# Performance work log

Hardware: AMD Instinct MI355X
Metric: run time of the kernel (lower is better)

The kernel has to match this reference:

```python
import jax, jax.numpy as jnp
import numpy as np

B, T, C, H = 4, 2048, 1024, 16


def setup_inputs() -> dict:
    key = jax.random.key(0)
    k1, k2, k3 = jax.random.split(key, 3)
    x = jax.random.normal(k1, (B, T, C), dtype=jnp.float32)
    Wqkv = jax.random.normal(k2, (C, 3 * C), dtype=jnp.float32) * 0.02
    bqkv = jnp.zeros((3 * C,), dtype=jnp.float32)
    Wproj = jax.random.normal(k3, (C, C), dtype=jnp.float32) * 0.02
    bproj = jnp.zeros((C,), dtype=jnp.float32)
    return {"x": x, "Wqkv": Wqkv, "bqkv": bqkv, "Wproj": Wproj, "bproj": bproj}


def reference(x, Wqkv, bqkv, Wproj, bproj):
    Bx, Tx, Cx = x.shape
    head = Cx // H
    qkv = x @ Wqkv + bqkv                      # [B,T,3C]
    q, k, v = jnp.split(qkv, 3, axis=-1)
    q = q.reshape(Bx, Tx, H, head)
    k = k.reshape(Bx, Tx, H, head)
    v = v.reshape(Bx, Tx, H, head)
    scale = 1.0 / jnp.sqrt(jnp.asarray(head, dtype=x.dtype))
    scores = jnp.einsum('bqhd,bkhd->bhqk', q, k) * scale   # [B,H,T,T]
    causal = jnp.tril(jnp.ones((Tx, Tx), dtype=bool))       # [T,T]
    neg = jnp.finfo(x.dtype).min
    scores = jnp.where(causal[None, None, :, :], scores, neg)
    probs = jax.nn.softmax(scores, axis=-1)
    y = jnp.einsum('bhqk,bkhd->bqhd', probs, v).reshape(Bx, Tx, Cx)
    return y @ Wproj + bproj
```

## Files before the change

kernel.cpp:

```cpp
#include <hip/hip_runtime.h>
#include <stdint.h>

#define BB 4
#define TT 2048
#define CC 1024
#define HH 16

typedef __bf16 bf16x8 __attribute__((ext_vector_type(8)));
typedef float f32x4 __attribute__((ext_vector_type(4)));
typedef float f32x16 __attribute__((ext_vector_type(16)));
typedef unsigned short ushort8 __attribute__((ext_vector_type(8)));
typedef unsigned short ushort4v __attribute__((ext_vector_type(4)));

__device__ __forceinline__ unsigned short f2b(float f) {
    union { float f; unsigned u; } v; v.f = f;
    unsigned r = v.u + 0x7FFFu + ((v.u >> 16) & 1u);
    return (unsigned short)(r >> 16);
}
__device__ __forceinline__ unsigned pack2(float a, float b) {
    union { float f; unsigned u; } ua, ub; ua.f = a; ub.f = b;
    return __builtin_amdgcn_perm(ub.u + 0x8000u, ua.u + 0x8000u, 0x07060302u);
}
__device__ __forceinline__ float fexp2(float x) {
#if __has_builtin(__builtin_amdgcn_exp2f)
    return __builtin_amdgcn_exp2f(x);
#else
    return exp2f(x);
#endif
}
#define LOG2E 1.4426950408889634f

#define ASYNC16(gp, lp) __builtin_amdgcn_global_load_lds( \
    (const __attribute__((address_space(1))) void*)(gp),  \
    (__attribute__((address_space(3))) void*)(lp), 16, 0, 0)

__global__ __launch_bounds__(256) void k_prep(const float* __restrict__ x,
                                              unsigned short* __restrict__ x16,
                                              const float* __restrict__ Wqkv,
                                              unsigned short* __restrict__ wqkvT,
                                              const float* __restrict__ Wproj,
                                              unsigned short* __restrict__ wprojT) {
    const int bid = blockIdx.x;
    const int t = threadIdx.x;
    if (bid < 8192) {
        int i = (bid * 256 + t) * 4;
        float4 v = *(const float4*)(x + i);
        ushort4v o;
        o.x = f2b(v.x); o.y = f2b(v.y); o.z = f2b(v.z); o.w = f2b(v.w);
        *(ushort4v*)(x16 + i) = o;
        return;
    }
    __shared__ float tile[32][33];
    const float* in; unsigned short* out; int R, Cc, bx, by;
    if (bid < 11264) {
        int u = bid - 8192;
        in = Wqkv; out = wqkvT; R = CC; Cc = 3 * CC;
        bx = (u % 96) * 32; by = (u / 96) * 32;
    } else {
        int u = bid - 11264;
        in = Wproj; out = wprojT; R = CC; Cc = CC;
        bx = (u & 31) * 32; by = (u >> 5) * 32;
    }
    int tx = t & 31, ty = t >> 5;
    for (int i = 0; i < 32; i += 8)
        tile[ty + i][tx] = in[(size_t)(by + ty + i) * Cc + bx + tx];
    __syncthreads();
    for (int i = 0; i < 32; i += 8)
        out[(size_t)(bx + ty + i) * R + by + tx] = f2b(tile[tx][ty + i]);
}

#define QSCALE 0.125f

__global__ __launch_bounds__(256, 3) void k_gemmqkv128(const unsigned short* __restrict__ A,
                                                       const unsigned short* __restrict__ Bt,
                                                       const float* __restrict__ bias,
                                                       unsigned short* __restrict__ qo,
                                                       unsigned short* __restrict__ ko,
                                                       unsigned short* __restrict__ vo,
                                                       int M, int N, int K) {
    __shared__ unsigned short sm[3 * 8192];
    const int t = threadIdx.x;
    const int lane = t & 63;
    const int c = lane & 15, qd = lane >> 4;
    const int wave = t >> 6;
    const int wr = (wave >> 1) * 64, wc = (wave & 1) * 64;
    const int bm = blockIdx.x * 128, bn = blockIdx.y * 128;

    f32x4 acc[4][4] = {};

    const int srow = t >> 2;
    const int sch = (t & 3) ^ ((t >> 3) & 3);
    const unsigned short* Ap = A + (size_t)(bm + srow) * K + sch * 8;
    const unsigned short* Bp = Bt + (size_t)(bn + srow) * K + sch * 8;
    const int fch = qd ^ ((c >> 1) & 3);
    const int NT = K >> 5;

#define QSTG(buf, tt_) do {                                                \
        const unsigned short* ga_ = Ap + (size_t)(tt_) * 32;               \
        const unsigned short* gb_ = Bp + (size_t)(tt_) * 32;               \
        ASYNC16(ga_,                  &sm[(buf) * 8192 + t * 8]);          \
        ASYNC16(ga_ + (size_t)64 * K, &sm[(buf) * 8192 + 2048 + t * 8]);   \
        ASYNC16(gb_,                  &sm[(buf) * 8192 + 4096 + t * 8]);   \
        ASYNC16(gb_ + (size_t)64 * K, &sm[(buf) * 8192 + 6144 + t * 8]);   \
    } while (0)

    QSTG(0, 0);
    QSTG(1, 1);
    asm volatile("s_waitcnt vmcnt(4)" ::: "memory");
    __builtin_amdgcn_s_barrier();

    int bc = 0, b1 = 1, bs = 2;
    for (int tt = 0; tt < NT; ++tt) {
        const unsigned short* Ab = &sm[bc * 8192];
        const unsigned short* Bb = &sm[bc * 8192 + 4096];
        bf16x8 bf_[4], af[4];

        if (tt + 2 < NT) QSTG(bs, tt + 2);
#pragma unroll
        for (int j = 0; j < 4; j++)
            bf_[j] = *(const bf16x8*)&Bb[(wc + j * 16 + c) * 32 + fch * 8];
#pragma unroll
        for (int i = 0; i < 4; i++)
            af[i] = *(const bf16x8*)&Ab[(wr + i * 16 + c) * 32 + fch * 8];
        if (tt + 2 < NT) {
            asm volatile("s_waitcnt vmcnt(4)" ::: "memory");
        } else if (tt + 1 < NT) {
            asm volatile("s_waitcnt vmcnt(0)" ::: "memory");
        }
        __builtin_amdgcn_s_barrier();
        asm volatile("s_waitcnt lgkmcnt(0)" ::: "memory");
        __builtin_amdgcn_sched_barrier(0);
        __builtin_amdgcn_s_setprio(1);
#pragma unroll
        for (int i = 0; i < 4; i++)
#pragma unroll
            for (int j = 0; j < 4; j++)
                acc[i][j] = __builtin_amdgcn_mfma_f32_16x16x32_bf16(af[i], bf_[j], acc[i][j], 0, 0, 0);
        __builtin_amdgcn_s_setprio(0);
        __builtin_amdgcn_s_barrier();

        int tmp = bc; bc = b1; b1 = bs; bs = tmp;
    }
#undef QSTG

#pragma unroll
    for (int j = 0; j < 4; j++) {
        float bv = bias[bn + wc + j * 16 + c];
#pragma unroll
        for (int i = 0; i < 4; i++)
#pragma unroll
            for (int r = 0; r < 4; r++)
                acc[i][j][r] += bv;
    }

    if (bn < 2048) {
        unsigned short* dst = (bn < 1024) ? qo : ko;
        const int dcol0 = (bn < 1024) ? bn : bn - 1024;
        const float sc = (bn < 1024) ? QSCALE : 1.0f;
        for (int p = 0; p < 2; p++) {
            __syncthreads();
            for (int ii = 0; ii < 2; ii++) {
                int i = 2 * p + ii;
                int lr0 = (wr >> 1) + ii * 16 + qd * 4;
                for (int j = 0; j < 4; j++) {
                    int col = wc + j * 16 + c;
                    for (int r = 0; r < 4; r++)
                        sm[(lr0 + r) * 136 + col] = f2b(acc[i][j][r] * sc);
                }
            }
            __syncthreads();
            for (int op = 0; op < 4; op++) {
                int lr = (t >> 4) + op * 16;
                int ch = (t & 15) * 8;
                ushort8 v = *(ushort8*)&sm[lr * 136 + ch];
                int grow = bm + (lr >> 5) * 64 + 32 * p + (lr & 31);
                *(ushort8*)&dst[(size_t)grow * 1024 + dcol0 + ch] = v;
            }
        }
    } else {
        const int bseg = bm >> 11;
        const int bmt = bm & 2047;
        for (int p = 0; p < 2; p++) {
            __syncthreads();
            for (int jj = 0; jj < 2; jj++) {
                int j = 2 * p + jj;
                int dl = (wc >> 1) + jj * 16 + c;
                for (int i = 0; i < 4; i++) {
                    int tl = wr + i * 16 + qd * 4;
                    ushort4v pk;
                    pk.x = f2b(acc[i][j][0]); pk.y = f2b(acc[i][j][1]);
                    pk.z = f2b(acc[i][j][2]); pk.w = f2b(acc[i][j][3]);
                    *(ushort4v*)&sm[dl * 136 + tl] = pk;
                }
            }
            __syncthreads();
            for (int op = 0; op < 4; op++) {
                int dl = (t >> 4) + op * 16;
                int ch = (t & 15) * 8;
                ushort8 v = *(ushort8*)&sm[dl * 136 + ch];
                int d = (bn - 2048) + (dl >> 5) * 64 + 32 * p + (dl & 31);
                *(ushort8*)&vo[((size_t)bseg * 1024 + d) * 2048 + bmt + ch] = v;
            }
        }
    }
}

__global__ __launch_bounds__(256, 3) void k_gemmproj128(const unsigned short* __restrict__ A,
                                                        const unsigned short* __restrict__ Bt,
                                                        const float* __restrict__ bias,
                                                        float* __restrict__ outf,
                                                        int M, int N, int K) {
    __shared__ unsigned short sm[3 * 8192];
    const int t = threadIdx.x;
    const int lane = t & 63;
    const int c = lane & 15, qd = lane >> 4;
    const int wave = t >> 6;
    const int wr = (wave >> 1) * 64, wc = (wave & 1) * 64;
    const int bm = blockIdx.x * 128, bn = blockIdx.y * 128;

    f32x4 acc[4][4] = {};

    const int srow = t >> 2;
    const int sch = (t & 3) ^ ((t >> 3) & 3);
    const unsigned short* Ap = A + (size_t)(bm + srow) * K + sch * 8;
    const unsigned short* Bp = Bt + (size_t)(bn + srow) * K + sch * 8;
    const int fch = qd ^ ((c >> 1) & 3);
    const int NT = K >> 5;

#define PSTG_A(buf, tt_) do {                                              \
        const unsigned short* ga_ = Ap + (size_t)(tt_) * 32;               \
        ASYNC16(ga_,                  &sm[(buf) * 8192 + t * 8]);          \
        ASYNC16(ga_ + (size_t)64 * K, &sm[(buf) * 8192 + 2048 + t * 8]);   \
    } while (0)
#define PSTG_B(buf, tt_) do {                                              \
        const unsigned short* gb_ = Bp + (size_t)(tt_) * 32;               \
        ASYNC16(gb_,                  &sm[(buf) * 8192 + 4096 + t * 8]);   \
        ASYNC16(gb_ + (size_t)64 * K, &sm[(buf) * 8192 + 6144 + t * 8]);   \
    } while (0)

    PSTG_A(0, 0); PSTG_B(0, 0);
    PSTG_A(1, 1); PSTG_B(1, 1);
    asm volatile("s_waitcnt vmcnt(4)" ::: "memory");
    __builtin_amdgcn_s_barrier();

    int bc = 0, b1 = 1, bs = 2;
    for (int tt = 0; tt < NT; ++tt) {
        const unsigned short* Ab = &sm[bc * 8192];
        const unsigned short* Bb = &sm[bc * 8192 + 4096];
        bf16x8 bf_[4], af[2];

        if (tt + 2 < NT) PSTG_A(bs, tt + 2);
#pragma unroll
        for (int j = 0; j < 4; j++)
            bf_[j] = *(const bf16x8*)&Bb[(wc + j * 16 + c) * 32 + fch * 8];
#pragma unroll
        for (int i = 0; i < 2; i++)
            af[i] = *(const bf16x8*)&Ab[(wr + i * 16 + c) * 32 + fch * 8];
        __builtin_amdgcn_s_barrier();
        asm volatile("s_waitcnt lgkmcnt(0)" ::: "memory");
        __builtin_amdgcn_sched_barrier(0);
        __builtin_amdgcn_s_setprio(1);
#pragma unroll
        for (int i = 0; i < 2; i++)
#pragma unroll
            for (int j = 0; j < 4; j++)
                acc[i][j] = __builtin_amdgcn_mfma_f32_16x16x32_bf16(af[i], bf_[j], acc[i][j], 0, 0, 0);
        __builtin_amdgcn_s_setprio(0);
        __builtin_amdgcn_s_barrier();

        if (tt + 2 < NT) PSTG_B(bs, tt + 2);
#pragma unroll
        for (int i = 0; i < 2; i++)
            af[i] = *(const bf16x8*)&Ab[(wr + 32 + i * 16 + c) * 32 + fch * 8];
        if (tt + 2 < NT) {
            asm volatile("s_waitcnt vmcnt(4)" ::: "memory");
        } else if (tt + 1 < NT) {
            asm volatile("s_waitcnt vmcnt(0)" ::: "memory");
        }
        __builtin_amdgcn_s_barrier();
        asm volatile("s_waitcnt lgkmcnt(0)" ::: "memory");
        __builtin_amdgcn_sched_barrier(0);
        __builtin_amdgcn_s_setprio(1);
#pragma unroll
        for (int i = 0; i < 2; i++)
#pragma unroll
            for (int j = 0; j < 4; j++)
                acc[i + 2][j] = __builtin_amdgcn_mfma_f32_16x16x32_bf16(af[i], bf_[j], acc[i + 2][j], 0, 0, 0);
        __builtin_amdgcn_s_setprio(0);
        __builtin_amdgcn_s_barrier();

        int tmp = bc; bc = b1; b1 = bs; bs = tmp;
    }
#undef PSTG_A
#undef PSTG_B

#pragma unroll
    for (int j = 0; j < 4; j++) {
        float bv = bias[bn + wc + j * 16 + c];
#pragma unroll
        for (int i = 0; i < 4; i++)
#pragma unroll
            for (int r = 0; r < 4; r++)
                acc[i][j][r] += bv;
    }

    float* smf = (float*)sm;
    for (int p = 0; p < 4; p++) {
        __syncthreads();
        int lr0 = (wr >> 2) + qd * 4;
        for (int j = 0; j < 4; j++) {
            int col = wc + j * 16 + c;
            for (int r = 0; r < 4; r++)
                smf[(lr0 + r) * 132 + col] = acc[p][j][r];
        }
        __syncthreads();
        for (int op = 0; op < 4; op++) {
            int lr = (t >> 5) + op * 8;
            int ch = (t & 31) * 4;
            float4 v = *(float4*)&smf[lr * 132 + ch];
            int grow = bm + (lr >> 4) * 64 + 16 * p + (lr & 15);
            *(float4*)&outf[(size_t)grow * N + bn + ch] = v;
        }
    }
}

__global__ __launch_bounds__(512, 4) void k_attn(const unsigned short* __restrict__ q16,
                                                 const unsigned short* __restrict__ k16,
                                                 const unsigned short* __restrict__ vT16,
                                                 unsigned short* __restrict__ y16) {
    const int bid = blockIdx.x;
    const int xcd = bid & 7;
    const int jj0 = bid >> 3;
    const int gid = xcd * 8 + (jj0 >> 3);
    const int u   = jj0 & 7;
    const int base = (u & 1) ? (7 - (u >> 1)) : (u >> 1);
    const int h = gid & 15, b = gid >> 4;
    const int qiA = base, qiB = 15 - base;
    __shared__ unsigned short smem[256 * 72];
    unsigned short* q_s = smem;
    const int t = threadIdx.x, lane = t & 63, wave = t >> 6;
    const int l31 = lane & 31, hl = lane >> 5;
    const int tile = wave >> 2;
    const int qw = (wave & 3) * 32;
    const int qi = tile ? qiB : qiA;

    {
        int row = t >> 1, c32 = (t & 1) * 32;
        int qtile = row >> 7, rr = row & 127;
        int qsrc_i = qtile ? qiB : qiA;
        const unsigned short* src = q16 + ((size_t)(b * TT + qsrc_i * 128 + rr)) * CC + h * 64 + c32;
        ushort8 v0 = *(const ushort8*)(src);
        ushort8 v1 = *(const ushort8*)(src + 8);
        ushort8 v2 = *(const ushort8*)(src + 16);
        ushort8 v3 = *(const ushort8*)(src + 24);
        *(ushort8*)&q_s[row * 72 + c32] = v0;
        *(ushort8*)&q_s[row * 72 + c32 + 8] = v1;
        *(ushort8*)&q_s[row * 72 + c32 + 16] = v2;
        *(ushort8*)&q_s[row * 72 + c32 + 24] = v3;
    }
    __syncthreads();
    bf16x8 qf[4];
    for (int s = 0; s < 4; s++)
        qf[s] = *(const bf16x8*)&q_s[(tile * 128 + qw + l31) * 72 + s * 16 + hl * 8];

    f32x16 oacc[2] = {};
    float l = 0.f;
    const float negmnl = -8.0f * LOG2E;
    const int qmaxw = qi * 128 + qw + 31;
    const int qminw = qi * 128 + qw;
    const int qg = qi * 128 + qw + l31;
    const int jn = 2 * qiB + 2;
    const unsigned short* kbase = k16 + (size_t)b * TT * CC + h * 64;
    const unsigned short* vbase = vT16 + (((size_t)b * 16 + h) * 64) * TT;

    const int t2 = t & 255;
    const int row = t2 >> 2, c16 = (t2 & 3) * 16;
    const bool doK = (t < 256);
    const unsigned short* ssrc = (doK ? (kbase + (size_t)row * CC)
                                      : (vbase + (size_t)row * TT)) + c16;
    unsigned short* sdst0 = smem + (doK ? 0 : 64 * 72) + row * 72 + c16;
    const size_t sstep = doK ? (size_t)64 * CC : (size_t)64;
    ushort8 sa = *(const ushort8*)ssrc, sb = *(const ushort8*)(ssrc + 8);

    __syncthreads();
    *(ushort8*)sdst0 = sa;
    *(ushort8*)(sdst0 + 8) = sb;
    {
        const unsigned short* nx = ssrc + sstep;
        sa = *(const ushort8*)nx; sb = *(const ushort8*)(nx + 8);
    }
    __syncthreads();

    for (int j = 0; j < jn; j++) {
        if (j + 1 < jn) {
            unsigned short* d = sdst0 + ((j + 1) & 1) * 9216;
            *(ushort8*)d = sa;
            *(ushort8*)(d + 8) = sb;
        }
        if (j + 2 < jn) {
            const unsigned short* nx = ssrc + (size_t)(j + 2) * sstep;
            sa = *(const ushort8*)nx; sb = *(const ushort8*)(nx + 8);
        }

        if (j * 64 <= qmaxw) {
            const unsigned short* k_s = smem + (j & 1) * 9216;
            const unsigned short* vt_s = k_s + 64 * 72;

            f32x16 sacc[2] = {};
            for (int c2 = 0; c2 < 2; c2++)
                for (int s = 0; s < 4; s++) {
                    bf16x8 kf = *(const bf16x8*)&k_s[(c2 * 32 + l31) * 72 + s * 16 + hl * 8];
                    sacc[c2] = __builtin_amdgcn_mfma_f32_32x32x16_bf16(kf, qf[s], sacc[c2], 0, 0, 0);
                }

            if (j * 64 + 63 > qminw) {
                for (int c2 = 0; c2 < 2; c2++)
                    for (int r = 0; r < 16; r++) {
                        int kvg = j * 64 + c2 * 32 + (r & 3) + 8 * (r >> 2) + 4 * hl;
                        if (kvg > qg) sacc[c2][r] = -1e30f;
                    }
            }

            float sum = 0.f;
            unsigned pg[2][4][2];
            for (int c2 = 0; c2 < 2; c2++)
                for (int g = 0; g < 4; g++) {
                    float p0 = fexp2(fmaf(sacc[c2][g * 4 + 0], LOG2E, negmnl));
                    float p1 = fexp2(fmaf(sacc[c2][g * 4 + 1], LOG2E, negmnl));
                    float p2 = fexp2(fmaf(sacc[c2][g * 4 + 2], LOG2E, negmnl));
                    float p3 = fexp2(fmaf(sacc[c2][g * 4 + 3], LOG2E, negmnl));
                    sum += (p0 + p1) + (p2 + p3);
                    pg[c2][g][0] = pack2(p0, p1);
                    pg[c2][g][1] = pack2(p2, p3);
                }
            sum += __shfl_xor(sum, 32, 64);
            l += sum;

            bf16x8 pf[4];
            for (int c2 = 0; c2 < 2; c2++)
                for (int pr = 0; pr < 2; pr++) {
                    unsigned a0 = pg[c2][2 * pr][0], b0 = pg[c2][2 * pr + 1][0];
                    unsigned a1 = pg[c2][2 * pr][1], b1 = pg[c2][2 * pr + 1][1];
                    asm("v_permlane32_swap_b32 %0, %1" : "+v"(a0), "+v"(b0));
                    asm("v_permlane32_swap_b32 %0, %1" : "+v"(a1), "+v"(b1));
                    union { unsigned u[4]; bf16x8 v; } fr;
                    fr.u[0] = a0; fr.u[1] = a1; fr.u[2] = b0; fr.u[3] = b1;
                    pf[c2 * 2 + pr] = fr.v;
                }

            for (int s = 0; s < 4; s++)
                for (int c2o = 0; c2o < 2; c2o++) {
                    bf16x8 vf = *(const bf16x8*)&vt_s[(c2o * 32 + l31) * 72 + s * 16 + hl * 8];
                    oacc[c2o] = __builtin_amdgcn_mfma_f32_32x32x16_bf16(vf, pf[s], oacc[c2o], 0, 0, 0);
                }
        }

        __syncthreads();
    }

    float rl = 1.0f / l;
    size_t rowb = ((size_t)b * TT + qg) * CC + h * 64;
    for (int c2 = 0; c2 < 2; c2++)
        for (int g = 0; g < 4; g++) {
            ushort4v pk;
            pk.x = f2b(oacc[c2][g * 4 + 0] * rl);
            pk.y = f2b(oacc[c2][g * 4 + 1] * rl);
            pk.z = f2b(oacc[c2][g * 4 + 2] * rl);
            pk.w = f2b(oacc[c2][g * 4 + 3] * rl);
            *(ushort4v*)&y16[rowb + c2 * 32 + g * 8 + hl * 4] = pk;
        }
}

extern "C" void kernel_launch(void* const* d_in, const int* in_sizes, int n_in,
                              void* d_out, int out_size, void* d_ws, size_t ws_size,
                              hipStream_t stream) {
    const float* x     = (const float*)d_in[0];
    const float* Wqkv  = (const float*)d_in[1];
    const float* bqkv  = (const float*)d_in[2];
    const float* Wproj = (const float*)d_in[3];
    const float* bproj = (const float*)d_in[4];
    float* out = (float*)d_out;

    const int M = BB * TT;
    unsigned short* x16    = (unsigned short*)d_ws;
    unsigned short* y16    = x16;
    unsigned short* wqkvT  = x16 + (size_t)M * CC;
    unsigned short* wprojT = wqkvT + (size_t)3 * CC * CC;
    unsigned short* q16    = wprojT + (size_t)CC * CC;
    unsigned short* k16    = q16 + (size_t)M * CC;
    unsigned short* vT16   = k16 + (size_t)M * CC;

    k_prep<<<12288, 256, 0, stream>>>(x, x16, Wqkv, wqkvT, Wproj, wprojT);
    k_gemmqkv128<<<dim3(M / 128, 3 * CC / 128), 256, 0, stream>>>(x16, wqkvT, bqkv,
                                                                  q16, k16, vT16, M, 3 * CC, CC);
    k_attn<<<dim3(512), 512, 0, stream>>>(q16, k16, vT16, y16);
    k_gemmproj128<<<dim3(M / 128, CC / 128), 256, 0, stream>>>(y16, wprojT, bproj, out, M, CC, CC);
}
```

Baseline: 230.8 us.

## Switch QKV GEMM to K=64 double-buffered tiles with 8-chunk XOR swizzle

The QKV projection GEMM moves from a triple-buffered K=32 pipeline to a double-buffered K=64 pipeline. Each iteration now stages 64-wide tiles with a new 8-chunk XOR swizzle and issues two rounds of MFMAs per barrier, which halves the number of loop iterations and barriers. LDS use per block doubles to 64KB and launch bounds drop to 2 blocks per CU. The cost is reduced occupancy and prefetch only one stage ahead, so less load latency is hidden.

```diff
diff --git a/kernel.cpp b/kernel.cpp
--- a/kernel.cpp
+++ b/kernel.cpp
@@ -71,63 +71,70 @@
 
 #define QSCALE 0.125f
 
-__global__ __launch_bounds__(256, 3) void k_gemmqkv128(const unsigned short* __restrict__ A,
+__global__ __launch_bounds__(256, 2) void k_gemmqkv128(const unsigned short* __restrict__ A,
                                                        const unsigned short* __restrict__ Bt,
                                                        const float* __restrict__ bias,
                                                        unsigned short* __restrict__ qo,
                                                        unsigned short* __restrict__ ko,
                                                        unsigned short* __restrict__ vo,
                                                        int M, int N, int K) {
-    __shared__ unsigned short sm[3 * 8192];
+    __shared__ unsigned short sm[2 * 16384];
     const int t = threadIdx.x;
     const int lane = t & 63;
     const int c = lane & 15, qd = lane >> 4;
+    const int cx = c & 7;
     const int wave = t >> 6;
     const int wr = (wave >> 1) * 64, wc = (wave & 1) * 64;
     const int bm = blockIdx.x * 128, bn = blockIdx.y * 128;
 
     f32x4 acc[4][4] = {};
 
-    const int srow = t >> 2;
-    const int sch = (t & 3) ^ ((t >> 3) & 3);
+    const int srow = t >> 3;
+    const int sch = (t & 7) ^ (srow & 7);
     const unsigned short* Ap = A + (size_t)(bm + srow) * K + sch * 8;
     const unsigned short* Bp = Bt + (size_t)(bn + srow) * K + sch * 8;
-    const int fch = qd ^ ((c >> 1) & 3);
-    const int NT = K >> 5;
-
-#define QSTG(buf, tt_) do {                                                \
-        const unsigned short* ga_ = Ap + (size_t)(tt_) * 32;               \
-        const unsigned short* gb_ = Bp + (size_t)(tt_) * 32;               \
-        ASYNC16(ga_,                  &sm[(buf) * 8192 + t * 8]);          \
-        ASYNC16(ga_ + (size_t)64 * K, &sm[(buf) * 8192 + 2048 + t * 8]);   \
-        ASYNC16(gb_,                  &sm[(buf) * 8192 + 4096 + t * 8]);   \
-        ASYNC16(gb_ + (size_t)64 * K, &sm[(buf) * 8192 + 6144 + t * 8]);   \
+    const int NT2 = K >> 6;
+
+#define QSTG64(buf, tt_) do {                                               \
+        const unsigned short* ga_ = Ap + (size_t)(tt_) * 64;                \
+        const unsigned short* gb_ = Bp + (size_t)(tt_) * 64;                \
+        ASYNC16(ga_,                  &sm[(buf) * 16384 + t * 8]);          \
+        ASYNC16(ga_ + (size_t)32 * K, &sm[(buf) * 16384 + 2048 + t * 8]);   \
+        ASYNC16(ga_ + (size_t)64 * K, &sm[(buf) * 16384 + 4096 + t * 8]);   \
+        ASYNC16(ga_ + (size_t)96 * K, &sm[(buf) * 16384 + 6144 + t * 8]);   \
+        ASYNC16(gb_,                  &sm[(buf) * 16384 + 8192 + t * 8]);   \
+        ASYNC16(gb_ + (size_t)32 * K, &sm[(buf) * 16384 + 10240 + t * 8]);  \
+        ASYNC16(gb_ + (size_t)64 * K, &sm[(buf) * 16384 + 12288 + t * 8]);  \
+        ASYNC16(gb_ + (size_t)96 * K, &sm[(buf) * 16384 + 14336 + t * 8]);  \
     } while (0)
 
-    QSTG(0, 0);
-    QSTG(1, 1);
-    asm volatile("s_waitcnt vmcnt(4)" ::: "memory");
-    __builtin_amdgcn_s_barrier();
-
-    int bc = 0, b1 = 1, bs = 2;
-    for (int tt = 0; tt < NT; ++tt) {
-        const unsigned short* Ab = &sm[bc * 8192];
-        const unsigned short* Bb = &sm[bc * 8192 + 4096];
-        bf16x8 bf_[4], af[4];
-
-        if (tt + 2 < NT) QSTG(bs, tt + 2);
-#pragma unroll
-        for (int j = 0; j < 4; j++)
-            bf_[j] = *(const bf16x8*)&Bb[(wc + j * 16 + c) * 32 + fch * 8];
-#pragma unroll
-        for (int i = 0; i < 4; i++)
-            af[i] = *(const bf16x8*)&Ab[(wr + i * 16 + c) * 32 + fch * 8];
-        if (tt + 2 < NT) {
-            asm volatile("s_waitcnt vmcnt(4)" ::: "memory");
-        } else if (tt + 1 < NT) {
+    QSTG64(0, 0);
+
+    int cur = 0;
+    for (int tt = 0; tt < NT2; ++tt) {
+        __builtin_amdgcn_s_barrier();
+        if (tt + 1 < NT2) {
+            QSTG64(cur ^ 1, tt + 1);
+            asm volatile("s_waitcnt vmcnt(8)" ::: "memory");
+        } else {
             asm volatile("s_waitcnt vmcnt(0)" ::: "memory");
         }
-        __builtin_amdgcn_s_barrier();
+
+        const unsigned short* Ab = &sm[cur * 16384];
+        const unsigned short* Bb = &sm[cur * 16384 + 8192];
+        bf16x8 af0[4], af1[4], bf0[4], bf1[4];
+#pragma unroll
+        for (int i = 0; i < 4; i++) {
+            int r = (wr + i * 16 + c) * 64;
+            af0[i] = *(const bf16x8*)&Ab[r + ((qd) ^ cx) * 8];
+            af1[i] = *(const bf16x8*)&Ab[r + ((4 + qd) ^ cx) * 8];
+        }
+#pragma unroll
+        for (int j = 0; j < 4; j++) {
+            int r = (wc + j * 16 + c) * 64;
+            bf0[j] = *(const bf16x8*)&Bb[r + ((qd) ^ cx) * 8];
+            bf1[j] = *(const bf16x8*)&Bb[r + ((4 + qd) ^ cx) * 8];
+        }
         asm volatile("s_waitcnt lgkmcnt(0)" ::: "memory");
         __builtin_amdgcn_sched_barrier(0);
         __builtin_amdgcn_s_setprio(1);
@@ -135,13 +142,17 @@
         for (int i = 0; i < 4; i++)
 #pragma unroll
             for (int j = 0; j < 4; j++)
-                acc[i][j] = __builtin_amdgcn_mfma_f32_16x16x32_bf16(af[i], bf_[j], acc[i][j], 0, 0, 0);
+                acc[i][j] = __builtin_amdgcn_mfma_f32_16x16x32_bf16(af0[i], bf0[j], acc[i][j], 0, 0, 0);
+#pragma unroll
+        for (int i = 0; i < 4; i++)
+#pragma unroll
+            for (int j = 0; j < 4; j++)
+                acc[i][j] = __builtin_amdgcn_mfma_f32_16x16x32_bf16(af1[i], bf1[j], acc[i][j], 0, 0, 0);
         __builtin_amdgcn_s_setprio(0);
-        __builtin_amdgcn_s_barrier();
-
-        int tmp = bc; bc = b1; b1 = bs; bs = tmp;
-    }
-#undef QSTG
+
+        cur ^= 1;
+    }
+#undef QSTG64
 
 #pragma unroll
     for (int j = 0; j < 4; j++) {
```

Result: faster. 225.2 us, median of 2 (-2.4%).
